# Optimization experiments

Measured on AMD Instinct MI355X. Metric: run time of the kernel, lower is better.

## Reference

```python
import jax, jax.numpy as jnp
import numpy as np

B, N = 4096, 1024


def setup_inputs() -> dict:
    key = jax.random.key(0)
    k1, k2 = jax.random.split(key)
    cors = 0.1 * jax.random.normal(k1, (B, N, 3), dtype=jnp.float32)  # predicted correspondences/offsets
    p_src = jax.random.normal(k2, (B, N, 3), dtype=jnp.float32)       # source point cloud
    return {"cors": cors, "p_src": p_src}


def reference(cors, p_src):
    # p_pred = p_src + cors  (target points implied by correspondences)
    p_pred = p_src + cors
    # centroids over the point dimension: [B, 1, 3]
    src_centroid = jnp.mean(p_src, axis=1, keepdims=True)
    pred_centroid = jnp.mean(p_pred, axis=1, keepdims=True)
    src_trans = p_src - src_centroid
    pred_trans = p_pred - pred_centroid
    # 3x3 cross-covariance per batch: h = src_trans^T @ pred_trans  -> [B, 3, 3]
    h = jnp.einsum('bnd,bne->bde', src_trans, pred_trans)
    # tf.linalg.svd returns s, u, v with h = u diag(s) v^T; jnp returns u, s, vh with vh = v^T
    u, s, vh = jnp.linalg.svd(h, full_matrices=False)
    # r_est = v @ u^T = (u @ vh)^T
    r_est = jnp.swapaxes(jnp.matmul(u, vh), -1, -2)  # [B, 3, 3]
    # t_est = -r_est @ src_centroid^T + pred_centroid^T  -> [B, 3, 1]
    t_est = -jnp.matmul(r_est, jnp.swapaxes(src_centroid, -1, -2)) + jnp.swapaxes(pred_centroid, -1, -2)
    g_top = jnp.concatenate([r_est, t_est], axis=2)  # [B, 3, 4]
    last_row = jnp.broadcast_to(
        jnp.array([[[0.0, 0.0, 0.0, 1.0]]], dtype=g_top.dtype), (g_top.shape[0], 1, 4)
    )
    return jnp.concatenate([g_top, last_row], axis=1)  # [B, 4, 4]
```

## Files before the change

### kernel.cpp

```cpp
#include <hip/hip_runtime.h>


constexpr int NPTS    = 1024;
constexpr int THREADS = 256;
constexpr int NF4     = NPTS * 3 / 4;
constexpr int BPB     = 4;

__global__ __launch_bounds__(THREADS) void svd_layer_kernel(
    const float* __restrict__ cors,
    const float* __restrict__ p_src,
    float* __restrict__ out)
{
    __shared__ float4 lds_s[NF4];
    __shared__ float4 lds_c[NF4];
    __shared__ float  red[4][15];
    __shared__ float  allS[BPB][15];

    const int t = threadIdx.x;
    const int wave = t >> 6, lane = t & 63;
    const int b0 = blockIdx.x * BPB;

    const float4* s4 = reinterpret_cast<const float4*>(p_src) + (size_t)b0 * NF4;
    const float4* c4 = reinterpret_cast<const float4*>(cors)  + (size_t)b0 * NF4;

    float4 a0 = s4[t], a1 = s4[t + 256], a2 = s4[t + 512];
    float4 d0 = c4[t], d1 = c4[t + 256], d2 = c4[t + 512];

    for (int k = 0; k < BPB; ++k) {
        lds_s[t] = a0; lds_s[t + 256] = a1; lds_s[t + 512] = a2;
        lds_c[t] = d0; lds_c[t + 256] = d1; lds_c[t + 512] = d2;
        __syncthreads();

        if (k + 1 < BPB) {
            const float4* sn = s4 + (size_t)(k + 1) * NF4;
            const float4* cn = c4 + (size_t)(k + 1) * NF4;
            a0 = sn[t]; a1 = sn[t + 256]; a2 = sn[t + 512];
            d0 = cn[t]; d1 = cn[t + 256]; d2 = cn[t + 512];
        }

        const float4 t0 = lds_s[t*3+0], t1 = lds_s[t*3+1], t2 = lds_s[t*3+2];
        const float4 u0 = lds_c[t*3+0], u1 = lds_c[t*3+1], u2 = lds_c[t*3+2];

        const float sx[4] = {t0.x, t0.w, t1.z, t2.y};
        const float sy[4] = {t0.y, t1.x, t1.w, t2.z};
        const float sz[4] = {t0.z, t1.y, t2.x, t2.w};
        const float px[4] = {sx[0]+u0.x, sx[1]+u0.w, sx[2]+u1.z, sx[3]+u2.y};
        const float py[4] = {sy[0]+u0.y, sy[1]+u1.x, sy[2]+u1.w, sy[3]+u2.z};
        const float pz[4] = {sz[0]+u0.z, sz[1]+u1.y, sz[2]+u2.x, sz[3]+u2.w};

        float acc[15];
        #pragma unroll
        for (int i = 0; i < 15; ++i) acc[i] = 0.f;
        #pragma unroll
        for (int q = 0; q < 4; ++q) {
            acc[0]  += sx[q]; acc[1]  += sy[q]; acc[2]  += sz[q];
            acc[3]  += px[q]; acc[4]  += py[q]; acc[5]  += pz[q];
            acc[6]  += sx[q]*px[q]; acc[7]  += sx[q]*py[q]; acc[8]  += sx[q]*pz[q];
            acc[9]  += sy[q]*px[q]; acc[10] += sy[q]*py[q]; acc[11] += sy[q]*pz[q];
            acc[12] += sz[q]*px[q]; acc[13] += sz[q]*py[q]; acc[14] += sz[q]*pz[q];
        }

        #pragma unroll
        for (int off = 32; off > 0; off >>= 1) {
            #pragma unroll
            for (int i = 0; i < 15; ++i) acc[i] += __shfl_down(acc[i], off, 64);
        }

        if (lane == 0) {
            #pragma unroll
            for (int i = 0; i < 15; ++i) red[wave][i] = acc[i];
        }
        __syncthreads();
        if (t < 15) allS[k][t] = red[0][t] + red[1][t] + red[2][t] + red[3][t];
    }

    __syncthreads();
    if (t >= BPB) return;

    float S[15];
    #pragma unroll
    for (int i = 0; i < 15; ++i) S[i] = allS[t][i];

    const float invN = 1.0f / (float)NPTS;
    const float cs[3] = {S[0]*invN, S[1]*invN, S[2]*invN};
    const float cp[3] = {S[3]*invN, S[4]*invN, S[5]*invN};

    float Hm[3][3];
    #pragma unroll
    for (int i = 0; i < 3; ++i)
        #pragma unroll
        for (int j = 0; j < 3; ++j)
            Hm[i][j] = S[6 + i*3 + j] - (float)NPTS * cs[i] * cp[j];

    float K[3][3];
    #pragma unroll
    for (int i = 0; i < 3; ++i)
        #pragma unroll
        for (int j = 0; j < 3; ++j)
            K[i][j] = Hm[0][i]*Hm[0][j] + Hm[1][i]*Hm[1][j] + Hm[2][i]*Hm[2][j];

    const float tr3 = (K[0][0] + K[1][1] + K[2][2]) * (1.0f/3.0f);
    const float is  = 1.0f / fmaxf(tr3, 1e-30f);

    float Y[3][3], Z[3][3];
    #pragma unroll
    for (int i = 0; i < 3; ++i)
        #pragma unroll
        for (int j = 0; j < 3; ++j) {
            Y[i][j] = K[i][j] * is;
            Z[i][j] = (i == j) ? 1.0f : 0.0f;
        }

    #pragma unroll
    for (int it = 0; it < 6; ++it) {
        float W[3][3];
        #pragma unroll
        for (int i = 0; i < 3; ++i)
            #pragma unroll
            for (int j = 0; j < 3; ++j) {
                float w = Z[i][0]*Y[0][j] + Z[i][1]*Y[1][j] + Z[i][2]*Y[2][j];
                W[i][j] = ((i == j) ? 1.5f : 0.0f) - 0.5f * w;
            }
        float Yn[3][3], Zn[3][3];
        #pragma unroll
        for (int i = 0; i < 3; ++i)
            #pragma unroll
            for (int j = 0; j < 3; ++j) {
                Yn[i][j] = Y[i][0]*W[0][j] + Y[i][1]*W[1][j] + Y[i][2]*W[2][j];
                Zn[i][j] = W[i][0]*Z[0][j] + W[i][1]*Z[1][j] + W[i][2]*Z[2][j];
            }
        #pragma unroll
        for (int i = 0; i < 3; ++i)
            #pragma unroll
            for (int j = 0; j < 3; ++j) { Y[i][j] = Yn[i][j]; Z[i][j] = Zn[i][j]; }
    }

    const float rs = rsqrtf(fmaxf(tr3, 1e-30f));
    float R[3][3];
    #pragma unroll
    for (int i = 0; i < 3; ++i)
        #pragma unroll
        for (int j = 0; j < 3; ++j)
            R[i][j] = (Z[i][0]*Hm[j][0] + Z[i][1]*Hm[j][1] + Z[i][2]*Hm[j][2]) * rs;

    const float tx = cp[0] - (R[0][0]*cs[0] + R[0][1]*cs[1] + R[0][2]*cs[2]);
    const float ty = cp[1] - (R[1][0]*cs[0] + R[1][1]*cs[1] + R[1][2]*cs[2]);
    const float tz = cp[2] - (R[2][0]*cs[0] + R[2][1]*cs[1] + R[2][2]*cs[2]);

    float4* o4 = reinterpret_cast<float4*>(out + (size_t)(b0 + t) * 16);
    o4[0] = make_float4(R[0][0], R[0][1], R[0][2], tx);
    o4[1] = make_float4(R[1][0], R[1][1], R[1][2], ty);
    o4[2] = make_float4(R[2][0], R[2][1], R[2][2], tz);
    o4[3] = make_float4(0.f, 0.f, 0.f, 1.f);
}

extern "C" void kernel_launch(void* const* d_in, const int* in_sizes, int n_in,
                              void* d_out, int out_size, void* d_ws, size_t ws_size,
                              hipStream_t stream)
{
    const float* cors  = (const float*)d_in[0];
    const float* p_src = (const float*)d_in[1];
    float* out = (float*)d_out;
    const int B = in_sizes[0] / (NPTS * 3);
    const int grid = B / BPB;
    hipLaunchKernelGGL(svd_layer_kernel, dim3(grid), dim3(THREADS), 0, stream,
                       cors, p_src, out);
}
```

Baseline: 118.8 us.

## Use DPP quad reduction with transposed shuffle tree and fewer batches per block

Replaces the 15-value shuffle-down wave reduction with two DPP quad-xor steps, then spreads the 15 sums across the four lanes of each quad so only 4 values go through the remaining xor-shuffle steps. Per-wave partial sums are written straight to shared memory and summed by the final thread, which drops the per-iteration cross-wave reduction barrier. A barrier is added after the LDS reads so the next iteration can overwrite the buffers safely. Batches per block drop from 4 to 2, doubling the grid and shortening each block's serial loop.

```diff
diff --git a/kernel.cpp b/kernel.cpp
--- a/kernel.cpp
+++ b/kernel.cpp
@@ -4,7 +4,16 @@
 constexpr int NPTS    = 1024;
 constexpr int THREADS = 256;
 constexpr int NF4     = NPTS * 3 / 4;
-constexpr int BPB     = 4;
+constexpr int BPB     = 2;
+
+__device__ __forceinline__ float dpp_qxor1(float x) {
+    int y = __builtin_amdgcn_update_dpp(0, __float_as_int(x), 0xB1, 0xF, 0xF, true);
+    return __int_as_float(y);
+}
+__device__ __forceinline__ float dpp_qxor2(float x) {
+    int y = __builtin_amdgcn_update_dpp(0, __float_as_int(x), 0x4E, 0xF, 0xF, true);
+    return __int_as_float(y);
+}
 
 __global__ __launch_bounds__(THREADS) void svd_layer_kernel(
     const float* __restrict__ cors,
@@ -13,8 +22,7 @@
 {
     __shared__ float4 lds_s[NF4];
     __shared__ float4 lds_c[NF4];
-    __shared__ float  red[4][15];
-    __shared__ float  allS[BPB][15];
+    __shared__ float  allS[BPB][4][16];
 
     const int t = threadIdx.x;
     const int wave = t >> 6, lane = t & 63;
@@ -40,6 +48,7 @@
 
         const float4 t0 = lds_s[t*3+0], t1 = lds_s[t*3+1], t2 = lds_s[t*3+2];
         const float4 u0 = lds_c[t*3+0], u1 = lds_c[t*3+1], u2 = lds_c[t*3+2];
+        __syncthreads();
 
         const float sx[4] = {t0.x, t0.w, t1.z, t2.y};
         const float sy[4] = {t0.y, t1.x, t1.w, t2.z};
@@ -61,17 +70,28 @@
         }
 
         #pragma unroll
-        for (int off = 32; off > 0; off >>= 1) {
-            #pragma unroll
-            for (int i = 0; i < 15; ++i) acc[i] += __shfl_down(acc[i], off, 64);
+        for (int i = 0; i < 15; ++i) acc[i] += dpp_qxor1(acc[i]);
+        #pragma unroll
+        for (int i = 0; i < 15; ++i) acc[i] += dpp_qxor2(acc[i]);
+
+        const int c = lane & 3;
+        float r0 = (c==0)?acc[0]:(c==1)?acc[4]:(c==2)?acc[8] :acc[12];
+        float r1 = (c==0)?acc[1]:(c==1)?acc[5]:(c==2)?acc[9] :acc[13];
+        float r2 = (c==0)?acc[2]:(c==1)?acc[6]:(c==2)?acc[10]:acc[14];
+        float r3 = (c==0)?acc[3]:(c==1)?acc[7]:(c==2)?acc[11]:0.f;
+
+        #pragma unroll
+        for (int off = 4; off <= 32; off <<= 1) {
+            r0 += __shfl_xor(r0, off, 64);
+            r1 += __shfl_xor(r1, off, 64);
+            r2 += __shfl_xor(r2, off, 64);
+            r3 += __shfl_xor(r3, off, 64);
         }
 
-        if (lane == 0) {
-            #pragma unroll
-            for (int i = 0; i < 15; ++i) red[wave][i] = acc[i];
+        if (lane < 4) {
+            float* dst = &allS[k][wave][lane * 4];
+            dst[0] = r0; dst[1] = r1; dst[2] = r2; dst[3] = r3;
         }
-        __syncthreads();
-        if (t < 15) allS[k][t] = red[0][t] + red[1][t] + red[2][t] + red[3][t];
     }
 
     __syncthreads();
@@ -79,7 +99,8 @@
 
     float S[15];
     #pragma unroll
-    for (int i = 0; i < 15; ++i) S[i] = allS[t][i];
+    for (int i = 0; i < 15; ++i)
+        S[i] = allS[t][0][i] + allS[t][1][i] + allS[t][2][i] + allS[t][3][i];
 
     const float invN = 1.0f / (float)NPTS;
     const float cs[3] = {S[0]*invN, S[1]*invN, S[2]*invN};
```

After: 116.5 us. About the same (-1.9%).
